# Kernel tuning notes

Hardware: AMD Instinct MI355X
Metric: run time of the kernel (lower is better)

## Reference

```python
import jax, jax.numpy as jnp
import numpy as np

H = 1024   # hidden_size
S = 1024   # seq_length
B = 32     # batch_size


def setup_inputs() -> dict:
    key = jax.random.key(0)
    k1, k2, k3, k4, k5, k6 = jax.random.split(key, 6)
    scale = 1.0 / np.sqrt(3 * H)
    return {
        "encoder_states": jax.random.normal(k1, (S, B, 2 * H), dtype=jnp.float32),
        "hidden": jax.random.normal(k2, (B, H), dtype=jnp.float32),
        "cell": jax.random.normal(k3, (B, H), dtype=jnp.float32),
        "W_attn": jax.random.normal(k4, (H, 3 * H), dtype=jnp.float32) * scale,
        "b_attn": jax.random.normal(k5, (H,), dtype=jnp.float32) * scale,
        "v_w": jax.random.normal(k6, (H,), dtype=jnp.float32) * (1.0 / np.sqrt(H)),
    }


def reference(encoder_states, hidden, cell, W_attn, b_attn, v_w):
    # cell is accepted by the original forward but unused.
    # Split the concat-linear into two projections (mathematically identical,
    # avoids materializing the repeated hidden + concat tensor):
    # cat((hidden_rep, enc), -1) @ W.T == hidden @ W[:, :H].T + enc @ W[:, H:].T
    W_h = W_attn[:, :H]          # [H, H]   multiplies decoder hidden
    W_e = W_attn[:, H:]          # [H, 2H]  multiplies encoder states
    enc = jnp.transpose(encoder_states, (1, 0, 2))          # [B, S, 2H]
    h_proj = hidden @ W_h.T + b_attn                         # [B, H], broadcast over S
    e_proj = jnp.einsum("bse,he->bsh", enc, W_e)             # [B, S, H]
    energy = jnp.tanh(h_proj[:, None, :] + e_proj)           # [B, S, H]
    attention = jnp.einsum("bsh,h->bs", energy, v_w)         # [B, S]
    return jax.nn.softmax(attention, axis=1)
```

## Files before the change

kernel.cpp:

```cpp
#include <hip/hip_runtime.h>

#define H 1024
#define S 1024
#define B 32
#define K2 2048

typedef unsigned short u16;
typedef __attribute__((ext_vector_type(8))) short short8;
typedef __attribute__((ext_vector_type(8))) unsigned short u16x8;
typedef __attribute__((ext_vector_type(4))) float floatx4;

__device__ __forceinline__ u16 f2bf(float f) {
  unsigned u = __float_as_uint(f);
  u += 0x7FFFu + ((u >> 16) & 1u);
  return (u16)(u >> 16);
}

__device__ __forceinline__ void gld_lds16(const u16* g, u16* l) {
  __builtin_amdgcn_global_load_lds(
      (const __attribute__((address_space(1))) unsigned int*)g,
      (__attribute__((address_space(3))) unsigned int*)l, 16, 0, 0);
}

__global__ void conv_enc_k(const float* __restrict__ src, u16* __restrict__ dst) {
  const int b = blockIdx.x >> 8;
  const int sc = blockIdx.x & 255;
  const int t = threadIdx.x * 8;
#pragma unroll
  for (int i = 0; i < 4; i++) {
    const int s = sc * 4 + i;
    const float* sp = src + ((size_t)s * B + b) * K2 + t;
    u16* dp = dst + ((size_t)b * S + s) * K2 + t;
    floatx4 x = *(const floatx4*)sp;
    floatx4 y = *(const floatx4*)(sp + 4);
    u16x8 o;
    o[0] = f2bf(x[0]); o[1] = f2bf(x[1]); o[2] = f2bf(x[2]); o[3] = f2bf(x[3]);
    o[4] = f2bf(y[0]); o[5] = f2bf(y[1]); o[6] = f2bf(y[2]); o[7] = f2bf(y[3]);
    *(u16x8*)dp = o;
  }
}

__global__ void conv_we_k(const float* __restrict__ W, u16* __restrict__ dst) {
  const int h = blockIdx.x;
  const int t = threadIdx.x * 8;
  const float* sp = W + (size_t)h * 3072 + H + t;
  u16* dp = dst + (size_t)h * K2 + t;
  floatx4 x = *(const floatx4*)sp;
  floatx4 y = *(const floatx4*)(sp + 4);
  u16x8 o;
  o[0] = f2bf(x[0]); o[1] = f2bf(x[1]); o[2] = f2bf(x[2]); o[3] = f2bf(x[3]);
  o[4] = f2bf(y[0]); o[5] = f2bf(y[1]); o[6] = f2bf(y[2]); o[7] = f2bf(y[3]);
  *(u16x8*)dp = o;
}

__global__ void hproj_k(const float* __restrict__ hidden, const float* __restrict__ W,
                        const float* __restrict__ b_attn, float* __restrict__ hp) {
  const int lane = threadIdx.x & 63;
  const int h = (blockIdx.x * blockDim.x + threadIdx.x) >> 6;
  float wr[16];
#pragma unroll
  for (int i = 0; i < 16; i++) wr[i] = W[(size_t)h * 3072 + lane + i * 64];
  for (int b = 0; b < B; b++) {
    float d = 0.f;
#pragma unroll
    for (int i = 0; i < 16; i++) d = fmaf(wr[i], hidden[b * H + lane + i * 64], d);
#pragma unroll
    for (int off = 32; off; off >>= 1) d += __shfl_xor(d, off);
    if (lane == 0) hp[b * H + h] = d + b_attn[h];
  }
}

#define BM 128
#define BN 128
#define BK 32

__global__ __launch_bounds__(256) void gemm_fused_k(
    const u16* __restrict__ A,
    const u16* __restrict__ Bw,
    const float* __restrict__ hp, const float* __restrict__ vw,
    float* __restrict__ attn) {
  __shared__ __align__(16) u16 sA[BM * BK];
  __shared__ __align__(16) u16 sB[BN * BK];
  const int tid = threadIdx.x;
  const int bid = blockIdx.x;
  const int ntile = bid >> 8;
  const int b = (bid & 255) >> 3;
  const int mtile = bid & 7;
  const int s0 = mtile * BM;
  const int h0 = ntile * BN;

  const int lane = tid & 63;
  const int wv = tid >> 6;
  const int wm = (wv >> 1) * 64;
  const int wn = (wv & 1) * 64;
  const int fr = lane & 15;
  const int kgrp = lane >> 4;

  const int lr = lane >> 2;
  const int sg = lane & 3;

  const u16* Ab = A + (size_t)(b * S + s0) * K2;
  const u16* Bb = Bw + (size_t)h0 * K2;

  floatx4 acc[4][4];
#pragma unroll
  for (int i = 0; i < 4; i++)
#pragma unroll
    for (int j = 0; j < 4; j++) acc[i][j] = (floatx4){0.f, 0.f, 0.f, 0.f};

  for (int k0 = 0; k0 < K2; k0 += BK) {
    __syncthreads();
#pragma unroll
    for (int p = 0; p < 2; p++) {
      const int rA = wv * 32 + p * 16 + lr;
      gld_lds16(Ab + (size_t)rA * K2 + k0 + (size_t)((sg ^ (rA & 3)) * 8),
                &sA[(wv * 32 + p * 16) * BK]);
      gld_lds16(Bb + (size_t)rA * K2 + k0 + (size_t)((sg ^ (rA & 3)) * 8),
                &sB[(wv * 32 + p * 16) * BK]);
    }
    __syncthreads();

    short8 af[4], bf[4];
#pragma unroll
    for (int mf = 0; mf < 4; mf++) {
      const int row = wm + mf * 16 + fr;
      af[mf] = *(const short8*)&sA[row * BK + (kgrp ^ (row & 3)) * 8];
    }
#pragma unroll
    for (int nf = 0; nf < 4; nf++) {
      const int row = wn + nf * 16 + fr;
      bf[nf] = *(const short8*)&sB[row * BK + (kgrp ^ (row & 3)) * 8];
    }
#pragma unroll
    for (int mf = 0; mf < 4; mf++)
#pragma unroll
      for (int nf = 0; nf < 4; nf++)
        acc[mf][nf] =
            __builtin_amdgcn_mfma_f32_16x16x32_bf16(af[mf], bf[nf], acc[mf][nf], 0, 0, 0);
  }

  const int col = fr;
  const int rgrp = lane >> 4;
  float hv[4], vv[4];
#pragma unroll
  for (int nf = 0; nf < 4; nf++) {
    const int h = h0 + wn + nf * 16 + col;
    hv[nf] = hp[b * H + h];
    vv[nf] = vw[h];
  }
#pragma unroll
  for (int mf = 0; mf < 4; mf++) {
#pragma unroll
    for (int r = 0; r < 4; r++) {
      float part = 0.f;
#pragma unroll
      for (int nf = 0; nf < 4; nf++) part += tanhf(acc[mf][nf][r] + hv[nf]) * vv[nf];
      part += __shfl_xor(part, 1);
      part += __shfl_xor(part, 2);
      part += __shfl_xor(part, 4);
      part += __shfl_xor(part, 8);
      if (col == 0)
        atomicAdd(&attn[b * S + s0 + wm + mf * 16 + rgrp * 4 + r], part);
    }
  }
}

__global__ void softmax_k(const float* __restrict__ attn, float* __restrict__ out) {
  __shared__ float red[8];
  const int b = blockIdx.x;
  const int tid = threadIdx.x;
  const float* row = attn + b * S;
  float v[4];
#pragma unroll
  for (int i = 0; i < 4; i++) v[i] = row[tid + i * 256];
  float m = fmaxf(fmaxf(v[0], v[1]), fmaxf(v[2], v[3]));
#pragma unroll
  for (int off = 32; off; off >>= 1) m = fmaxf(m, __shfl_xor(m, off));
  if ((tid & 63) == 0) red[tid >> 6] = m;
  __syncthreads();
  m = fmaxf(fmaxf(red[0], red[1]), fmaxf(red[2], red[3]));
  float e[4], sum = 0.f;
#pragma unroll
  for (int i = 0; i < 4; i++) { e[i] = __expf(v[i] - m); sum += e[i]; }
#pragma unroll
  for (int off = 32; off; off >>= 1) sum += __shfl_xor(sum, off);
  __syncthreads();
  if ((tid & 63) == 0) red[4 + (tid >> 6)] = sum;
  __syncthreads();
  sum = red[4] + red[5] + red[6] + red[7];
  const float inv = 1.0f / sum;
#pragma unroll
  for (int i = 0; i < 4; i++) out[b * S + tid + i * 256] = e[i] * inv;
}

extern "C" void kernel_launch(void* const* d_in, const int* in_sizes, int n_in,
                              void* d_out, int out_size, void* d_ws, size_t ws_size,
                              hipStream_t stream) {
  const float* enc    = (const float*)d_in[0];
  const float* hidden = (const float*)d_in[1];
  const float* W_attn = (const float*)d_in[3];
  const float* b_attn = (const float*)d_in[4];
  const float* v_w    = (const float*)d_in[5];
  float* out = (float*)d_out;

  char* ws = (char*)d_ws;
  float* attn = (float*)ws;
  float* hp   = (float*)(ws + 131072);
  u16* Web    = (u16*)(ws + 262144);
  u16* encb   = (u16*)(ws + 262144 + (size_t)H * K2 * 2);

  hipMemsetAsync(attn, 0, B * S * sizeof(float), stream);
  conv_enc_k<<<B * 256, 256, 0, stream>>>(enc, encb);
  conv_we_k<<<H, 256, 0, stream>>>(W_attn, Web);
  hproj_k<<<256, 256, 0, stream>>>(hidden, W_attn, b_attn, hp);
  gemm_fused_k<<<2048, 256, 0, stream>>>(encb, Web, hp, v_w, attn);
  softmax_k<<<B, 256, 0, stream>>>(attn, out);
}
```

Before: 611.6 us.

## Fuse encoder fp32-to-bf16 conversion into GEMM tile loads

Drops the standalone pass that converts and transposes the encoder states to bf16. The GEMM now loads fp32 encoder rows directly into LDS with a strided per-batch layout and converts them to bf16 fragments in registers before MFMA. This removes a full read and write of the large encoder tensor, but doubles the bytes per A tile and LDS usage, and adds conversion work in the inner loop. It also changes the B-tile swizzle pattern.

```diff
diff --git a/kernel.cpp b/kernel.cpp
--- a/kernel.cpp
+++ b/kernel.cpp
@@ -1,4 +1,5 @@
 #include <hip/hip_runtime.h>
+#include <hip/hip_bf16.h>
 
 #define H 1024
 #define S 1024
@@ -16,28 +17,24 @@
   return (u16)(u >> 16);
 }
 
-__device__ __forceinline__ void gld_lds16(const u16* g, u16* l) {
+__device__ __forceinline__ void gld_lds16(const void* g, void* l) {
   __builtin_amdgcn_global_load_lds(
       (const __attribute__((address_space(1))) unsigned int*)g,
       (__attribute__((address_space(3))) unsigned int*)l, 16, 0, 0);
 }
 
-__global__ void conv_enc_k(const float* __restrict__ src, u16* __restrict__ dst) {
-  const int b = blockIdx.x >> 8;
-  const int sc = blockIdx.x & 255;
-  const int t = threadIdx.x * 8;
-#pragma unroll
-  for (int i = 0; i < 4; i++) {
-    const int s = sc * 4 + i;
-    const float* sp = src + ((size_t)s * B + b) * K2 + t;
-    u16* dp = dst + ((size_t)b * S + s) * K2 + t;
-    floatx4 x = *(const floatx4*)sp;
-    floatx4 y = *(const floatx4*)(sp + 4);
-    u16x8 o;
-    o[0] = f2bf(x[0]); o[1] = f2bf(x[1]); o[2] = f2bf(x[2]); o[3] = f2bf(x[3]);
-    o[4] = f2bf(y[0]); o[5] = f2bf(y[1]); o[6] = f2bf(y[2]); o[7] = f2bf(y[3]);
-    *(u16x8*)dp = o;
-  }
+__device__ __forceinline__ unsigned cvt_pk(float lo, float hi) {
+  __hip_bfloat162 h = __float22bfloat162_rn(float2{lo, hi});
+  return *(unsigned*)&h;
+}
+
+__device__ __forceinline__ short8 mk_frag(floatx4 lo, floatx4 hi) {
+  union { unsigned u[4]; short8 s; } r;
+  r.u[0] = cvt_pk(lo[0], lo[1]);
+  r.u[1] = cvt_pk(lo[2], lo[3]);
+  r.u[2] = cvt_pk(hi[0], hi[1]);
+  r.u[3] = cvt_pk(hi[2], hi[3]);
+  return r.s;
 }
 
 __global__ void conv_we_k(const float* __restrict__ W, u16* __restrict__ dst) {
@@ -75,11 +72,11 @@
 #define BK 32
 
 __global__ __launch_bounds__(256) void gemm_fused_k(
-    const u16* __restrict__ A,
+    const float* __restrict__ enc,
     const u16* __restrict__ Bw,
     const float* __restrict__ hp, const float* __restrict__ vw,
     float* __restrict__ attn) {
-  __shared__ __align__(16) u16 sA[BM * BK];
+  __shared__ __align__(16) float sA[BM * 32];
   __shared__ __align__(16) u16 sB[BN * BK];
   const int tid = threadIdx.x;
   const int bid = blockIdx.x;
@@ -96,11 +93,8 @@
   const int fr = lane & 15;
   const int kgrp = lane >> 4;
 
-  const int lr = lane >> 2;
-  const int sg = lane & 3;
-
-  const u16* Ab = A + (size_t)(b * S + s0) * K2;
-  const u16* Bb = Bw + (size_t)h0 * K2;
+  const int lr8 = lane >> 3, sg8 = lane & 7;
+  const int lr4 = lane >> 2, sg4 = lane & 3;
 
   floatx4 acc[4][4];
 #pragma unroll
@@ -111,25 +105,32 @@
   for (int k0 = 0; k0 < K2; k0 += BK) {
     __syncthreads();
 #pragma unroll
+    for (int p = 0; p < 4; p++) {
+      const int r = wv * 32 + p * 8 + lr8;
+      gld_lds16(enc + ((size_t)(s0 + r) * B + b) * K2 + k0 + ((sg8 ^ (r & 7)) << 2),
+                (char*)sA + (wv * 32 + p * 8) * 128);
+    }
+#pragma unroll
     for (int p = 0; p < 2; p++) {
-      const int rA = wv * 32 + p * 16 + lr;
-      gld_lds16(Ab + (size_t)rA * K2 + k0 + (size_t)((sg ^ (rA & 3)) * 8),
-                &sA[(wv * 32 + p * 16) * BK]);
-      gld_lds16(Bb + (size_t)rA * K2 + k0 + (size_t)((sg ^ (rA & 3)) * 8),
-                &sB[(wv * 32 + p * 16) * BK]);
+      const int r = wv * 32 + p * 16 + lr4;
+      gld_lds16(Bw + (size_t)(h0 + r) * K2 + k0 + ((sg4 ^ ((r >> 1) & 3)) << 3),
+                (char*)sB + (wv * 32 + p * 16) * 64);
     }
     __syncthreads();
 
     short8 af[4], bf[4];
 #pragma unroll
     for (int mf = 0; mf < 4; mf++) {
-      const int row = wm + mf * 16 + fr;
-      af[mf] = *(const short8*)&sA[row * BK + (kgrp ^ (row & 3)) * 8];
+      const int R = wm + mf * 16 + fr;
+      const int f7 = R & 7;
+      floatx4 lo = *(const floatx4*)&sA[R * 32 + ((((kgrp << 1)) ^ f7) << 2)];
+      floatx4 hi = *(const floatx4*)&sA[R * 32 + ((((kgrp << 1) | 1) ^ f7) << 2)];
+      af[mf] = mk_frag(lo, hi);
     }
 #pragma unroll
     for (int nf = 0; nf < 4; nf++) {
-      const int row = wn + nf * 16 + fr;
-      bf[nf] = *(const short8*)&sB[row * BK + (kgrp ^ (row & 3)) * 8];
+      const int R = wn + nf * 16 + fr;
+      bf[nf] = *(const short8*)&sB[R * BK + ((kgrp ^ ((R >> 1) & 3)) << 3)];
     }
 #pragma unroll
     for (int mf = 0; mf < 4; mf++)
@@ -207,12 +208,10 @@
   float* attn = (float*)ws;
   float* hp   = (float*)(ws + 131072);
   u16* Web    = (u16*)(ws + 262144);
-  u16* encb   = (u16*)(ws + 262144 + (size_t)H * K2 * 2);
 
   hipMemsetAsync(attn, 0, B * S * sizeof(float), stream);
-  conv_enc_k<<<B * 256, 256, 0, stream>>>(enc, encb);
   conv_we_k<<<H, 256, 0, stream>>>(W_attn, Web);
   hproj_k<<<256, 256, 0, stream>>>(hidden, W_attn, b_attn, hp);
-  gemm_fused_k<<<2048, 256, 0, stream>>>(encb, Web, hp, v_w, attn);
+  gemm_fused_k<<<2048, 256, 0, stream>>>(enc, Web, hp, v_w, attn);
   softmax_k<<<B, 256, 0, stream>>>(attn, out);
 }
```

Measured after the change: 607.8 us. About the same (-0.6%).
